# Performance work log

Measured on AMD Instinct MI355X. Metric: run time of the kernel, lower is better.

The kernel has to match this reference:

```python
import jax, jax.numpy as jnp
import numpy as np

N, E, F_IN, H = 50000, 800000, 2, 128
S, G = 5000, 64  # num subgraphs, num graphs (static segment counts)
N_EXTRA_CONVS = 3  # num_layers - 1


def setup_inputs() -> dict:
    key = jax.random.key(0)
    ks = jax.random.split(key, 16)
    inv = lambda f: 1.0 / np.sqrt(f)
    return {
        "x": jax.random.normal(ks[0], (N, F_IN), dtype=jnp.float32),
        "edge_index": jax.random.randint(ks[1], (2, E), 0, N),
        "node_to_subgraph": jax.random.randint(ks[2], (N,), 0, S),
        "subgraph_to_graph": jax.random.randint(ks[3], (S,), 0, G),
        "W1a": jax.random.normal(ks[4], (F_IN, H), dtype=jnp.float32) * inv(F_IN),
        "b1a": jnp.zeros((H,), jnp.float32),
        "W1b": jax.random.normal(ks[5], (H, H), dtype=jnp.float32) * inv(H),
        "b1b": jnp.zeros((H,), jnp.float32),
        "convs_Wa": jax.random.normal(ks[6], (N_EXTRA_CONVS, H, H), dtype=jnp.float32) * inv(H),
        "convs_ba": jnp.zeros((N_EXTRA_CONVS, H), jnp.float32),
        "convs_Wb": jax.random.normal(ks[7], (N_EXTRA_CONVS, H, H), dtype=jnp.float32) * inv(H),
        "convs_bb": jnp.zeros((N_EXTRA_CONVS, H), jnp.float32),
        "lin1_W": jax.random.normal(ks[8], (H, H), dtype=jnp.float32) * inv(H),
        "lin1_b": jnp.zeros((H,), jnp.float32),
        "lin2_W": jax.random.normal(ks[9], (H, H), dtype=jnp.float32) * inv(H),
        "lin2_b": jnp.zeros((H,), jnp.float32),
    }


def reference(x, edge_index, node_to_subgraph, subgraph_to_graph,
              W1a, b1a, W1b, b1b, convs_Wa, convs_ba, convs_Wb, convs_bb,
              lin1_W, lin1_b, lin2_W, lin2_b):
    src, dst = edge_index[0], edge_index[1]

    def gin_conv(h, Wa, ba, Wb, bb):
        # GIN aggregation (eps=0): h_i + sum over incoming neighbors
        aggr = jax.ops.segment_sum(h[src], dst, num_segments=N)
        h = h + aggr
        h = jax.nn.relu(h @ Wa + ba)
        return jax.nn.relu(h @ Wb + bb)

    h = gin_conv(x, W1a, b1a, W1b, b1b)
    for i in range(N_EXTRA_CONVS):
        h = gin_conv(h, convs_Wa[i], convs_ba[i], convs_Wb[i], convs_bb[i])

    # nested pooling: nodes -> subgraphs -> graphs
    h = jax.ops.segment_sum(h, node_to_subgraph, num_segments=S)
    h = jax.ops.segment_sum(h, subgraph_to_graph, num_segments=G)

    h = jax.nn.relu(h @ lin1_W + lin1_b)
    # dropout is identity in eval mode
    h = h @ lin2_W + lin2_b
    return jax.nn.log_softmax(h, axis=1)
```

## Files before the change

### kernel.cpp

```cpp
#include <hip/hip_runtime.h>
#include <cstddef>

#define N_NODES  50000
#define N_EDGES  800000
#define HDIM     128
#define SSUB     5000
#define GGRAPH   64
#define FILL_Q   416
#define LDSW     136

#define EB 3125
#define NB 196
#define WB 448
#define SB 20

typedef unsigned int uint;
typedef unsigned short ushort;
typedef __attribute__((ext_vector_type(8))) short bf16x8;
typedef __attribute__((ext_vector_type(4))) float f32x4;
typedef __attribute__((ext_vector_type(16))) float f32x16;

__device__ __forceinline__ float bflo(uint v) { return __uint_as_float(v << 16); }
__device__ __forceinline__ float bfhi(uint v) { return __uint_as_float(v & 0xffff0000u); }
__device__ __forceinline__ uint packbf(float lo, float hi) {
    uint a = __float_as_uint(lo), b = __float_as_uint(hi);
    a = (a + 0x7fff + ((a >> 16) & 1)) >> 16;
    b = (b + 0x7fff + ((b >> 16) & 1)) & 0xffff0000u;
    return a | b;
}
__device__ __forceinline__ ushort bf16of(float f) {
    uint a = __float_as_uint(f);
    a = (a + 0x7fff + ((a >> 16) & 1)) >> 16;
    return (ushort)a;
}


__global__ __launch_bounds__(256) void k_hist_all(const int* __restrict__ dst,
                                                  const int* __restrict__ n2s,
                                                  int* __restrict__ cnt,
                                                  int* __restrict__ rank,
                                                  int* __restrict__ scnt,
                                                  int* __restrict__ srank,
                                                  const float* __restrict__ W1b,
                                                  const float* __restrict__ cWa,
                                                  const float* __restrict__ cWb,
                                                  ushort* __restrict__ wt) {
    int b = blockIdx.x, t = threadIdx.x;
    if (b < EB) {
        int e = b * 256 + t;
        rank[e] = atomicAdd(&cnt[dst[e]], 1);
    } else if (b < EB + NB) {
        int i = (b - EB) * 256 + t;
        if (i < N_NODES) srank[i] = atomicAdd(&scnt[n2s[i]], 1);
    } else {
        int gid = (b - EB - NB) * 256 + t;
        int m = gid >> 14, r = gid & 16383;
        int n = r >> 7, k = r & 127;
        const float* Wsrc = (m == 0) ? W1b
                          : (m <= 3) ? cWa + (size_t)(m - 1) * 16384
                                     : cWb + (size_t)(m - 4) * 16384;
        wt[gid] = bf16of(Wsrc[k * 128 + n]);
    }
}


__global__ __launch_bounds__(256) void k_scan_reduce_all(const int* __restrict__ cnt,
                                                         const int* __restrict__ scnt,
                                                         int* __restrict__ bsum,
                                                         int* __restrict__ bsum2) {
    __shared__ int sd[256];
    int t = threadIdx.x;
    const int* srcp; int n, bb; int* dstp;
    if (blockIdx.x < NB) { srcp = cnt;  n = N_NODES; bb = blockIdx.x;      dstp = bsum;  }
    else                 { srcp = scnt; n = SSUB;    bb = blockIdx.x - NB; dstp = bsum2; }
    int idx = bb * 256 + t;
    sd[t] = (idx < n) ? srcp[idx] : 0;
    __syncthreads();
    for (int off = 128; off > 0; off >>= 1) {
        if (t < off) sd[t] += sd[t + off];
        __syncthreads();
    }
    if (t == 0) dstp[bb] = sd[0];
}

__global__ __launch_bounds__(256) void k_scan_top_all(const int* __restrict__ bsum,
                                                      int* __restrict__ boff,
                                                      const int* __restrict__ bsum2,
                                                      int* __restrict__ boff2) {
    __shared__ int sd[256];
    int t = threadIdx.x;
    sd[t] = (t < NB) ? bsum[t] : 0;
    __syncthreads();
    for (int off = 1; off < 256; off <<= 1) {
        int v = (t >= off) ? sd[t - off] : 0;
        __syncthreads();
        sd[t] += v;
        __syncthreads();
    }
    boff[t] = (t == 0) ? 0 : sd[t - 1];
    __syncthreads();
    sd[t] = (t < SB) ? bsum2[t] : 0;
    __syncthreads();
    for (int off = 1; off < 256; off <<= 1) {
        int v = (t >= off) ? sd[t - off] : 0;
        __syncthreads();
        sd[t] += v;
        __syncthreads();
    }
    if (t < 32) boff2[t] = (t == 0) ? 0 : sd[t - 1];
}

__global__ __launch_bounds__(256) void k_scan_final_all(const int* __restrict__ cnt,
                                                        const int* __restrict__ boff,
                                                        int* __restrict__ rowptr,
                                                        const int* __restrict__ scnt,
                                                        const int* __restrict__ boff2,
                                                        int* __restrict__ srowptr) {
    __shared__ int sd[256];
    int t = threadIdx.x;
    const int* srcp; const int* offp; int* outp; int n, total, bb;
    if (blockIdx.x < NB) { srcp = cnt;  offp = boff;  outp = rowptr;  n = N_NODES; total = N_EDGES; bb = blockIdx.x; }
    else                 { srcp = scnt; offp = boff2; outp = srowptr; n = SSUB;    total = N_NODES; bb = blockIdx.x - NB; }
    int idx = bb * 256 + t;
    int v = (idx < n) ? srcp[idx] : 0;
    sd[t] = v;
    __syncthreads();
    for (int off = 1; off < 256; off <<= 1) {
        int u = (t >= off) ? sd[t - off] : 0;
        __syncthreads();
        sd[t] += u;
        __syncthreads();
    }
    if (idx < n) outp[idx] = sd[t] - v + offp[bb];
    if (idx == 0) outp[n] = total;
}


__global__ __launch_bounds__(256) void k_fill_all(const int* __restrict__ src,
                                                  const int* __restrict__ dst,
                                                  const int* __restrict__ rank,
                                                  const int* __restrict__ rowptr,
                                                  int* __restrict__ csrc,
                                                  const int* __restrict__ n2s,
                                                  const int* __restrict__ srank,
                                                  const int* __restrict__ srowptr,
                                                  int* __restrict__ s2n) {
    if (blockIdx.x < 8 * FILL_Q) {
        int part = blockIdx.x & 7;
        int q = blockIdx.x >> 3;
        int lo = part * 6250, hi = lo + 6250;
        for (int e = q * 256 + threadIdx.x; e < N_EDGES; e += FILL_Q * 256) {
            int d = dst[e];
            if (d >= lo && d < hi) csrc[rowptr[d] + rank[e]] = src[e];
        }
    } else {
        int i = (blockIdx.x - 8 * FILL_Q) * 256 + threadIdx.x;
        if (i < N_NODES) s2n[srowptr[n2s[i]] + srank[i]] = i;
    }
}


__global__ __launch_bounds__(256) void k_layer1(const float2* __restrict__ x,
                                                const int* __restrict__ rowptr,
                                                const int* __restrict__ csrc,
                                                const float* __restrict__ W1a,
                                                const float* __restrict__ b1a,
                                                const ushort* __restrict__ WtA,
                                                const float* __restrict__ bA,
                                                ushort* __restrict__ hbout) {
    __shared__ ushort lds[64 * LDSW];
    const int tid = threadIdx.x, wave = tid >> 6, lane = tid & 63;
    const int quad = lane >> 4, l16 = lane & 15;
    const int nodeBase = blockIdx.x * 64;

    float2 wlo = ((const float2*)W1a)[lane];
    float2 whi = ((const float2*)W1a)[64 + lane];
    float2 bv  = ((const float2*)b1a)[lane];
    for (int n = wave * 16; n < wave * 16 + 16; ++n) {
        int gn = nodeBase + n;
        float tx = 0.f, ty = 0.f;
        if (gn < N_NODES) {
            int s = rowptr[gn], e = rowptr[gn + 1];
            for (int k = s + lane; k < e; k += 64) {
                float2 v = x[csrc[k]];
                tx += v.x; ty += v.y;
            }
        }
        for (int off = 32; off > 0; off >>= 1) {
            tx += __shfl_down(tx, off);
            ty += __shfl_down(ty, off);
        }
        tx = __shfl(tx, 0); ty = __shfl(ty, 0);
        uint pk = 0u;
        if (gn < N_NODES) {
            float2 sv = x[gn];
            tx += sv.x; ty += sv.y;
            float v0 = fmaf(tx, wlo.x, fmaf(ty, whi.x, bv.x));
            float v1 = fmaf(tx, wlo.y, fmaf(ty, whi.y, bv.y));
            pk = packbf(fmaxf(v0, 0.f), fmaxf(v1, 0.f));
        }
        *(uint*)(&lds[n * LDSW + 2 * lane]) = pk;
    }
    __syncthreads();

    f32x4 acc[8];
#pragma unroll
    for (int c = 0; c < 8; ++c) acc[c] = (f32x4){0.f, 0.f, 0.f, 0.f};
    const ushort* arow = lds + (wave * 16 + l16) * LDSW + quad * 8;
#pragma unroll
    for (int kk = 0; kk < 4; ++kk) {
        bf16x8 a = *(const bf16x8*)(arow + kk * 32);
#pragma unroll
        for (int c = 0; c < 8; ++c) {
            bf16x8 b = *(const bf16x8*)(WtA + (size_t)(c * 16 + l16) * 128 +
                                        kk * 32 + quad * 8);
            acc[c] = __builtin_amdgcn_mfma_f32_16x16x32_bf16(a, b, acc[c], 0, 0, 0);
        }
    }
#pragma unroll
    for (int r = 0; r < 4; ++r) {
        int row = nodeBase + wave * 16 + quad * 4 + r;
        if (row < N_NODES) {
#pragma unroll
            for (int c = 0; c < 8; ++c) {
                int col = c * 16 + l16;
                hbout[(size_t)row * 128 + col] = bf16of(fmaxf(acc[c][r] + bA[col], 0.f));
            }
        }
    }
}


__global__ __launch_bounds__(256) void k_aggr128_bf16(const uint* __restrict__ hb,
                                                      const int* __restrict__ rowptr,
                                                      const int* __restrict__ csrc,
                                                      uint* __restrict__ out) {
    int node = blockIdx.x * 4 + (threadIdx.x >> 6);
    int lane = threadIdx.x & 63;
    int s = rowptr[node], e = rowptr[node + 1];
    uint sv = hb[(size_t)node * 64 + lane];
    float ax0 = bflo(sv), ay0 = bfhi(sv);
    float ax1 = 0.f, ay1 = 0.f, ax2 = 0.f, ay2 = 0.f, ax3 = 0.f, ay3 = 0.f;
    for (int base = s; base < e; base += 64) {
        int cnt = e - base; if (cnt > 64) cnt = 64;
        int idx = csrc[base + ((lane < cnt) ? lane : 0)];
        int j = 0;
        for (; j + 7 < cnt; j += 8) {
            int s0 = __shfl(idx, j),     s1 = __shfl(idx, j + 1);
            int s2 = __shfl(idx, j + 2), s3 = __shfl(idx, j + 3);
            int s4 = __shfl(idx, j + 4), s5 = __shfl(idx, j + 5);
            int s6 = __shfl(idx, j + 6), s7 = __shfl(idx, j + 7);
            uint v0 = hb[(size_t)s0 * 64 + lane];
            uint v1 = hb[(size_t)s1 * 64 + lane];
            uint v2 = hb[(size_t)s2 * 64 + lane];
            uint v3 = hb[(size_t)s3 * 64 + lane];
            uint v4 = hb[(size_t)s4 * 64 + lane];
            uint v5 = hb[(size_t)s5 * 64 + lane];
            uint v6 = hb[(size_t)s6 * 64 + lane];
            uint v7 = hb[(size_t)s7 * 64 + lane];
            ax0 += bflo(v0); ay0 += bfhi(v0);
            ax1 += bflo(v1); ay1 += bfhi(v1);
            ax2 += bflo(v2); ay2 += bfhi(v2);
            ax3 += bflo(v3); ay3 += bfhi(v3);
            ax0 += bflo(v4); ay0 += bfhi(v4);
            ax1 += bflo(v5); ay1 += bfhi(v5);
            ax2 += bflo(v6); ay2 += bfhi(v6);
            ax3 += bflo(v7); ay3 += bfhi(v7);
        }
        for (; j < cnt; ++j) {
            int sj = __shfl(idx, j);
            uint v = hb[(size_t)sj * 64 + lane];
            ax0 += bflo(v); ay0 += bfhi(v);
        }
    }
    out[(size_t)node * 64 + lane] =
        packbf((ax0 + ax1) + (ax2 + ax3), (ay0 + ay1) + (ay2 + ay3));
}


__global__ __launch_bounds__(256) void k_mlp(const ushort* __restrict__ A,
                                             const ushort* __restrict__ WtA,
                                             const float* __restrict__ bA,
                                             const ushort* __restrict__ WtB,
                                             const float* __restrict__ bB,
                                             ushort* __restrict__ C, int nrows) {
    __shared__ ushort lds[128 * LDSW];
    const int tid = threadIdx.x;
    const int wave = tid >> 6, lane = tid & 63;
    const int l32 = lane & 31, hk = lane >> 5;
    const int colBase = wave * 32;
    const int rowBase = blockIdx.x * 128;

    {
        int r = tid >> 1;
        int halfu = (tid & 1) * 64;
        const uint4* gp = (const uint4*)(A + (size_t)(rowBase + r) * 128 + halfu);
        uint4* lp = (uint4*)(lds + r * LDSW + halfu);
        bool valid = (rowBase + r) < nrows;
#pragma unroll
        for (int q = 0; q < 8; ++q) {
            uint4 v = valid ? gp[q] : (uint4){0u, 0u, 0u, 0u};
            lp[q] = v;
        }
    }

    bf16x8 wa[8], wb[8];
#pragma unroll
    for (int kk = 0; kk < 8; ++kk) {
        wa[kk] = *(const bf16x8*)(WtA + (size_t)(colBase + l32) * 128 + kk * 16 + hk * 8);
        wb[kk] = *(const bf16x8*)(WtB + (size_t)(colBase + l32) * 128 + kk * 16 + hk * 8);
    }
    const float biasA = bA[colBase + l32];
    const float biasB = bB[colBase + l32];
    __syncthreads();

    f32x16 acc[4];
#pragma unroll
    for (int m = 0; m < 4; ++m)
#pragma unroll
        for (int r = 0; r < 16; ++r) acc[m][r] = 0.f;
#pragma unroll
    for (int m = 0; m < 4; ++m) {
        const ushort* arow = lds + (m * 32 + l32) * LDSW + hk * 8;
#pragma unroll
        for (int kk = 0; kk < 8; ++kk) {
            bf16x8 a = *(const bf16x8*)(arow + kk * 16);
            acc[m] = __builtin_amdgcn_mfma_f32_32x32x16_bf16(a, wa[kk], acc[m], 0, 0, 0);
        }
    }
    __syncthreads();

#pragma unroll
    for (int m = 0; m < 4; ++m) {
#pragma unroll
        for (int r = 0; r < 16; ++r) {
            int rl = (r & 3) + 8 * (r >> 2) + 4 * hk;
            lds[(m * 32 + rl) * LDSW + colBase + l32] =
                bf16of(fmaxf(acc[m][r] + biasA, 0.f));
        }
    }
    __syncthreads();

#pragma unroll
    for (int m = 0; m < 4; ++m)
#pragma unroll
        for (int r = 0; r < 16; ++r) acc[m][r] = 0.f;
#pragma unroll
    for (int m = 0; m < 4; ++m) {
        const ushort* arow = lds + (m * 32 + l32) * LDSW + hk * 8;
#pragma unroll
        for (int kk = 0; kk < 8; ++kk) {
            bf16x8 a = *(const bf16x8*)(arow + kk * 16);
            acc[m] = __builtin_amdgcn_mfma_f32_32x32x16_bf16(a, wb[kk], acc[m], 0, 0, 0);
        }
    }

#pragma unroll
    for (int m = 0; m < 4; ++m) {
#pragma unroll
        for (int r = 0; r < 16; ++r) {
            int rl = (r & 3) + 8 * (r >> 2) + 4 * hk;
            int row = rowBase + m * 32 + rl;
            if (row < nrows)
                C[(size_t)row * 128 + colBase + l32] =
                    bf16of(fmaxf(acc[m][r] + biasB, 0.f));
        }
    }
}


__global__ __launch_bounds__(256) void k_pool(const uint* __restrict__ hb,
                                              const int* __restrict__ srowptr,
                                              const int* __restrict__ s2n,
                                              const int* __restrict__ s2g,
                                              float* __restrict__ poolG) {
    int sg = blockIdx.x * 4 + (threadIdx.x >> 6);
    int lane = threadIdx.x & 63;
    int s = srowptr[sg], e = srowptr[sg + 1];
    float ax = 0.f, ay = 0.f;
    for (int base = s; base < e; base += 64) {
        int ec = e - base; if (ec > 64) ec = 64;
        int idx = s2n[base + ((lane < ec) ? lane : 0)];
        int j = 0;
        for (; j + 3 < ec; j += 4) {
            int n0 = __shfl(idx, j),     n1 = __shfl(idx, j + 1);
            int n2 = __shfl(idx, j + 2), n3 = __shfl(idx, j + 3);
            uint v0 = hb[(size_t)n0 * 64 + lane];
            uint v1 = hb[(size_t)n1 * 64 + lane];
            uint v2 = hb[(size_t)n2 * 64 + lane];
            uint v3 = hb[(size_t)n3 * 64 + lane];
            ax += bflo(v0) + bflo(v1) + bflo(v2) + bflo(v3);
            ay += bfhi(v0) + bfhi(v1) + bfhi(v2) + bfhi(v3);
        }
        for (; j < ec; ++j) {
            uint v = hb[(size_t)s2n[base + j] * 64 + lane];
            ax += bflo(v); ay += bfhi(v);
        }
    }
    int g = s2g[sg];
    atomicAdd(&poolG[(size_t)g * 128 + 2 * lane],     ax);
    atomicAdd(&poolG[(size_t)g * 128 + 2 * lane + 1], ay);
}


__global__ __launch_bounds__(128) void k_final(const float* __restrict__ poolG,
                                               const float* __restrict__ W1,
                                               const float* __restrict__ b1,
                                               const float* __restrict__ W2,
                                               const float* __restrict__ b2,
                                               float* __restrict__ out) {
    __shared__ float row[128];
    __shared__ float t1[128];
    __shared__ float red[128];
    int g = blockIdx.x, j = threadIdx.x;
    row[j] = poolG[g * 128 + j];
    __syncthreads();
    float s = b1[j];
    for (int k = 0; k < 128; ++k) s = fmaf(row[k], W1[k * 128 + j], s);
    t1[j] = fmaxf(s, 0.f);
    __syncthreads();
    float s2 = b2[j];
    for (int k = 0; k < 128; ++k) s2 = fmaf(t1[k], W2[k * 128 + j], s2);
    red[j] = s2;
    __syncthreads();
    for (int off = 64; off > 0; off >>= 1) {
        if (j < off) red[j] = fmaxf(red[j], red[j + off]);
        __syncthreads();
    }
    float m = red[0];
    __syncthreads();
    red[j] = expf(s2 - m);
    __syncthreads();
    for (int off = 64; off > 0; off >>= 1) {
        if (j < off) red[j] += red[j + off];
        __syncthreads();
    }
    float lse = m + logf(red[0]);
    out[g * 128 + j] = s2 - lse;
}


extern "C" void kernel_launch(void* const* d_in, const int* in_sizes, int n_in,
                              void* d_out, int out_size, void* d_ws, size_t ws_size,
                              hipStream_t stream) {
    (void)in_sizes; (void)n_in; (void)out_size; (void)ws_size;
    const float* x    = (const float*)d_in[0];
    const int*   ei   = (const int*)d_in[1];
    const int*   n2s  = (const int*)d_in[2];
    const int*   s2g  = (const int*)d_in[3];
    const float* W1a  = (const float*)d_in[4];
    const float* b1a  = (const float*)d_in[5];
    const float* W1b  = (const float*)d_in[6];
    const float* b1b  = (const float*)d_in[7];
    const float* cWa  = (const float*)d_in[8];
    const float* cba  = (const float*)d_in[9];
    const float* cWb  = (const float*)d_in[10];
    const float* cbb  = (const float*)d_in[11];
    const float* l1W  = (const float*)d_in[12];
    const float* l1b  = (const float*)d_in[13];
    const float* l2W  = (const float*)d_in[14];
    const float* l2b  = (const float*)d_in[15];
    float* out = (float*)d_out;

    uint*  hb      = (uint*)d_ws;
    uint*  habuf   = hb + (size_t)N_NODES * 64;
    int*   rowptr  = (int*)(habuf + (size_t)N_NODES * 64);
    int*   srowptr = rowptr + N_NODES + 2;
    int*   cnt     = srowptr + SSUB + 2;
    int*   scnt    = cnt + N_NODES;
    float* poolG   = (float*)(scnt + SSUB);
    int*   bsum    = (int*)(poolG + (size_t)GGRAPH * HDIM);
    int*   bsum2   = bsum + 256;
    int*   boff    = bsum2 + 32;
    int*   boff2   = boff + 256;
    int*   csrc    = boff2 + 32;
    int*   rank    = csrc + N_EDGES;
    int*   srank   = rank + N_EDGES;
    int*   s2n     = srank + N_NODES;
    ushort* wt     = (ushort*)(s2n + N_NODES);

    const int* srcA = ei;
    const int* dstA = ei + N_EDGES;
    const int nL1Blocks  = (N_NODES + 63) / 64;
    const int nMlpBlocks = (N_NODES + 127) / 128;

    hipMemsetAsync(cnt, 0, (size_t)(N_NODES + SSUB + GGRAPH * HDIM) * 4, stream);

    k_hist_all<<<EB + NB + WB, 256, 0, stream>>>(dstA, n2s, cnt, rank, scnt, srank,
                                                 W1b, cWa, cWb, wt);
    k_scan_reduce_all<<<NB + SB, 256, 0, stream>>>(cnt, scnt, bsum, bsum2);
    k_scan_top_all<<<1, 256, 0, stream>>>(bsum, boff, bsum2, boff2);
    k_scan_final_all<<<NB + SB, 256, 0, stream>>>(cnt, boff, rowptr, scnt, boff2, srowptr);
    k_fill_all<<<8 * FILL_Q + NB, 256, 0, stream>>>(srcA, dstA, rank, rowptr, csrc,
                                                    n2s, srank, srowptr, s2n);

    k_layer1<<<nL1Blocks, 256, 0, stream>>>((const float2*)x, rowptr, csrc,
                                            W1a, b1a, wt, b1b, (ushort*)hb);

    for (int i = 0; i < 3; ++i) {
        k_aggr128_bf16<<<N_NODES / 4, 256, 0, stream>>>(hb, rowptr, csrc, habuf);
        k_mlp<<<nMlpBlocks, 256, 0, stream>>>((const ushort*)habuf,
                                              wt + (size_t)(1 + i) * 16384,
                                              cba + i * HDIM,
                                              wt + (size_t)(4 + i) * 16384,
                                              cbb + i * HDIM,
                                              (ushort*)hb, N_NODES);
    }

    k_pool<<<SSUB / 4, 256, 0, stream>>>(hb, srowptr, s2n, s2g, poolG);
    k_final<<<GGRAPH, 128, 0, stream>>>(poolG, l1W, l1b, l2W, l2b, out);
}
```

Baseline: 373.8 us.

## Rework layer1 aggregation and MFMA tiling; halve MLP row tile

Layer-1 neighbor gathering now uses 4 threads per node for the whole block in one pass, where before it looped node by node with a full 64-lane wave reduction. The sums go to shared memory, and the first 128x128 matmul now uses 32x32x16 MFMA with register-held weights instead of 16x16x32 with weights reloaded from global. The MLP kernel drops its row tile from 128 to 64, doubling block count to raise occupancy and parallelism. The cost is that each block reloads the weights more often relative to the rows it computes.

```diff
diff --git a/kernel.cpp b/kernel.cpp
--- a/kernel.cpp
+++ b/kernel.cpp
@@ -17,7 +17,6 @@
 typedef unsigned int uint;
 typedef unsigned short ushort;
 typedef __attribute__((ext_vector_type(8))) short bf16x8;
-typedef __attribute__((ext_vector_type(4))) float f32x4;
 typedef __attribute__((ext_vector_type(16))) float f32x16;
 
 __device__ __forceinline__ float bflo(uint v) { return __uint_as_float(v << 16); }
@@ -169,63 +168,79 @@
                                                 const float* __restrict__ bA,
                                                 ushort* __restrict__ hbout) {
     __shared__ ushort lds[64 * LDSW];
+    __shared__ float2 sums[64];
     const int tid = threadIdx.x, wave = tid >> 6, lane = tid & 63;
-    const int quad = lane >> 4, l16 = lane & 15;
     const int nodeBase = blockIdx.x * 64;
 
-    float2 wlo = ((const float2*)W1a)[lane];
-    float2 whi = ((const float2*)W1a)[64 + lane];
-    float2 bv  = ((const float2*)b1a)[lane];
-    for (int n = wave * 16; n < wave * 16 + 16; ++n) {
-        int gn = nodeBase + n;
+    {
+        int nl = tid >> 2, sub = tid & 3;
+        int gn = nodeBase + nl;
         float tx = 0.f, ty = 0.f;
         if (gn < N_NODES) {
             int s = rowptr[gn], e = rowptr[gn + 1];
-            for (int k = s + lane; k < e; k += 64) {
+            for (int k = s + sub; k < e; k += 4) {
                 float2 v = x[csrc[k]];
                 tx += v.x; ty += v.y;
             }
         }
-        for (int off = 32; off > 0; off >>= 1) {
-            tx += __shfl_down(tx, off);
-            ty += __shfl_down(ty, off);
-        }
-        tx = __shfl(tx, 0); ty = __shfl(ty, 0);
-        uint pk = 0u;
-        if (gn < N_NODES) {
-            float2 sv = x[gn];
-            tx += sv.x; ty += sv.y;
-            float v0 = fmaf(tx, wlo.x, fmaf(ty, whi.x, bv.x));
-            float v1 = fmaf(tx, wlo.y, fmaf(ty, whi.y, bv.y));
-            pk = packbf(fmaxf(v0, 0.f), fmaxf(v1, 0.f));
-        }
-        *(uint*)(&lds[n * LDSW + 2 * lane]) = pk;
-    }
-    __syncthreads();
-
-    f32x4 acc[8];
-#pragma unroll
-    for (int c = 0; c < 8; ++c) acc[c] = (f32x4){0.f, 0.f, 0.f, 0.f};
-    const ushort* arow = lds + (wave * 16 + l16) * LDSW + quad * 8;
-#pragma unroll
-    for (int kk = 0; kk < 4; ++kk) {
-        bf16x8 a = *(const bf16x8*)(arow + kk * 32);
-#pragma unroll
-        for (int c = 0; c < 8; ++c) {
-            bf16x8 b = *(const bf16x8*)(WtA + (size_t)(c * 16 + l16) * 128 +
-                                        kk * 32 + quad * 8);
-            acc[c] = __builtin_amdgcn_mfma_f32_16x16x32_bf16(a, b, acc[c], 0, 0, 0);
-        }
-    }
-#pragma unroll
-    for (int r = 0; r < 4; ++r) {
-        int row = nodeBase + wave * 16 + quad * 4 + r;
-        if (row < N_NODES) {
-#pragma unroll
-            for (int c = 0; c < 8; ++c) {
-                int col = c * 16 + l16;
-                hbout[(size_t)row * 128 + col] = bf16of(fmaxf(acc[c][r] + bA[col], 0.f));
+        tx += __shfl_xor(tx, 1); ty += __shfl_xor(ty, 1);
+        tx += __shfl_xor(tx, 2); ty += __shfl_xor(ty, 2);
+        if (sub == 0) {
+            if (gn < N_NODES) {
+                float2 sv = x[gn];
+                sums[nl] = make_float2(tx + sv.x, ty + sv.y);
+            } else {
+                sums[nl] = make_float2(0.f, 0.f);
             }
+        }
+    }
+    __syncthreads();
+
+    {
+        float2 wlo = ((const float2*)W1a)[lane];
+        float2 whi = ((const float2*)W1a)[64 + lane];
+        float2 bv  = ((const float2*)b1a)[lane];
+        for (int n = wave * 16; n < wave * 16 + 16; ++n) {
+            float2 ts = sums[n];
+            float v0 = fmaf(ts.x, wlo.x, fmaf(ts.y, whi.x, bv.x));
+            float v1 = fmaf(ts.x, wlo.y, fmaf(ts.y, whi.y, bv.y));
+            *(uint*)(&lds[n * LDSW + 2 * lane]) = packbf(fmaxf(v0, 0.f), fmaxf(v1, 0.f));
+        }
+    }
+
+    const int l32 = lane & 31, hk = lane >> 5;
+    const int colBase = wave * 32;
+    bf16x8 wa[8];
+#pragma unroll
+    for (int kk = 0; kk < 8; ++kk)
+        wa[kk] = *(const bf16x8*)(WtA + (size_t)(colBase + l32) * 128 + kk * 16 + hk * 8);
+    const float biasA = bA[colBase + l32];
+    __syncthreads();
+
+    f32x16 acc[2];
+#pragma unroll
+    for (int m = 0; m < 2; ++m)
+#pragma unroll
+        for (int r = 0; r < 16; ++r) acc[m][r] = 0.f;
+#pragma unroll
+    for (int m = 0; m < 2; ++m) {
+        const ushort* arow = lds + (m * 32 + l32) * LDSW + hk * 8;
+#pragma unroll
+        for (int kk = 0; kk < 8; ++kk) {
+            bf16x8 a = *(const bf16x8*)(arow + kk * 16);
+            acc[m] = __builtin_amdgcn_mfma_f32_32x32x16_bf16(a, wa[kk], acc[m], 0, 0, 0);
+        }
+    }
+
+#pragma unroll
+    for (int m = 0; m < 2; ++m) {
+#pragma unroll
+        for (int r = 0; r < 16; ++r) {
+            int rl = (r & 3) + 8 * (r >> 2) + 4 * hk;
+            int row = nodeBase + m * 32 + rl;
+            if (row < N_NODES)
+                hbout[(size_t)row * 128 + colBase + l32] =
+                    bf16of(fmaxf(acc[m][r] + biasA, 0.f));
         }
     }
 }
@@ -284,21 +299,21 @@
                                              const ushort* __restrict__ WtB,
                                              const float* __restrict__ bB,
                                              ushort* __restrict__ C, int nrows) {
-    __shared__ ushort lds[128 * LDSW];
+    __shared__ ushort lds[64 * LDSW];
     const int tid = threadIdx.x;
     const int wave = tid >> 6, lane = tid & 63;
     const int l32 = lane & 31, hk = lane >> 5;
     const int colBase = wave * 32;
-    const int rowBase = blockIdx.x * 128;
+    const int rowBase = blockIdx.x * 64;
 
     {
-        int r = tid >> 1;
-        int halfu = (tid & 1) * 64;
-        const uint4* gp = (const uint4*)(A + (size_t)(rowBase + r) * 128 + halfu);
-        uint4* lp = (uint4*)(lds + r * LDSW + halfu);
+        int r = tid >> 2;
+        int qo = (tid & 3) * 32;
+        const uint4* gp = (const uint4*)(A + (size_t)(rowBase + r) * 128 + qo);
+        uint4* lp = (uint4*)(lds + r * LDSW + qo);
         bool valid = (rowBase + r) < nrows;
 #pragma unroll
-        for (int q = 0; q < 8; ++q) {
+        for (int q = 0; q < 4; ++q) {
             uint4 v = valid ? gp[q] : (uint4){0u, 0u, 0u, 0u};
             lp[q] = v;
         }
@@ -314,13 +329,13 @@
     const float biasB = bB[colBase + l32];
     __syncthreads();
 
-    f32x16 acc[4];
-#pragma unroll
-    for (int m = 0; m < 4; ++m)
+    f32x16 acc[2];
+#pragma unroll
+    for (int m = 0; m < 2; ++m)
 #pragma unroll
         for (int r = 0; r < 16; ++r) acc[m][r] = 0.f;
 #pragma unroll
-    for (int m = 0; m < 4; ++m) {
+    for (int m = 0; m < 2; ++m) {
         const ushort* arow = lds + (m * 32 + l32) * LDSW + hk * 8;
 #pragma unroll
         for (int kk = 0; kk < 8; ++kk) {
@@ -331,7 +346,7 @@
     __syncthreads();
 
 #pragma unroll
-    for (int m = 0; m < 4; ++m) {
+    for (int m = 0; m < 2; ++m) {
 #pragma unroll
         for (int r = 0; r < 16; ++r) {
             int rl = (r & 3) + 8 * (r >> 2) + 4 * hk;
@@ -342,11 +357,11 @@
     __syncthreads();
 
 #pragma unroll
-    for (int m = 0; m < 4; ++m)
+    for (int m = 0; m < 2; ++m)
 #pragma unroll
         for (int r = 0; r < 16; ++r) acc[m][r] = 0.f;
 #pragma unroll
-    for (int m = 0; m < 4; ++m) {
+    for (int m = 0; m < 2; ++m) {
         const ushort* arow = lds + (m * 32 + l32) * LDSW + hk * 8;
 #pragma unroll
         for (int kk = 0; kk < 8; ++kk) {
@@ -356,7 +371,7 @@
     }
 
 #pragma unroll
-    for (int m = 0; m < 4; ++m) {
+    for (int m = 0; m < 2; ++m) {
 #pragma unroll
         for (int r = 0; r < 16; ++r) {
             int rl = (r & 3) + 8 * (r >> 2) + 4 * hk;
@@ -481,8 +496,7 @@
 
     const int* srcA = ei;
     const int* dstA = ei + N_EDGES;
-    const int nL1Blocks  = (N_NODES + 63) / 64;
-    const int nMlpBlocks = (N_NODES + 127) / 128;
+    const int nTileBlocks = (N_NODES + 63) / 64;
 
     hipMemsetAsync(cnt, 0, (size_t)(N_NODES + SSUB + GGRAPH * HDIM) * 4, stream);
 
@@ -494,17 +508,17 @@
     k_fill_all<<<8 * FILL_Q + NB, 256, 0, stream>>>(srcA, dstA, rank, rowptr, csrc,
                                                     n2s, srank, srowptr, s2n);
 
-    k_layer1<<<nL1Blocks, 256, 0, stream>>>((const float2*)x, rowptr, csrc,
-                                            W1a, b1a, wt, b1b, (ushort*)hb);
+    k_layer1<<<nTileBlocks, 256, 0, stream>>>((const float2*)x, rowptr, csrc,
+                                              W1a, b1a, wt, b1b, (ushort*)hb);
 
     for (int i = 0; i < 3; ++i) {
         k_aggr128_bf16<<<N_NODES / 4, 256, 0, stream>>>(hb, rowptr, csrc, habuf);
-        k_mlp<<<nMlpBlocks, 256, 0, stream>>>((const ushort*)habuf,
-                                              wt + (size_t)(1 + i) * 16384,
-                                              cba + i * HDIM,
-                                              wt + (size_t)(4 + i) * 16384,
-                                              cbb + i * HDIM,
-                                              (ushort*)hb, N_NODES);
+        k_mlp<<<nTileBlocks, 256, 0, stream>>>((const ushort*)habuf,
+                                               wt + (size_t)(1 + i) * 16384,
+                                               cba + i * HDIM,
+                                               wt + (size_t)(4 + i) * 16384,
+                                               cbb + i * HDIM,
+                                               (ushort*)hb, N_NODES);
     }
 
     k_pool<<<SSUB / 4, 256, 0, stream>>>(hb, srowptr, s2n, s2g, poolG);
```

Measured after the change: 337.1 us. 9.8% less time.
